# Performance work log

Measured on AMD Instinct MI355X. Metric: run time of the kernel, lower is better.

## Reference

```python
import jax, jax.numpy as jnp
import numpy as np

N_NODES = 20000
N_EDGES = 320000
IN_CH = 512
HID = 128
HEADS = 4
OUT_CH = 256
NEG_SLOPE = 0.2


def _gat_layer(x, edge_index, W, a_src, a_dst, bias, heads, out_ch, concat):
    """PyG GATConv (add_self_loops=True, eval mode: no dropout).
    x: [N, F_in], edge_index: [2, E] (row 0 = src, row 1 = dst).
    Returns (out, alpha) with alpha: [E+N, heads].
    """
    N = x.shape[0]
    h = (x @ W).reshape(N, heads, out_ch)                      # [N, H, C]
    loops = jnp.arange(N, dtype=edge_index.dtype)
    src = jnp.concatenate([edge_index[0], loops])
    dst = jnp.concatenate([edge_index[1], loops])
    a_s = jnp.einsum('nhc,hc->nh', h, a_src)                   # [N, H]
    a_d = jnp.einsum('nhc,hc->nh', h, a_dst)
    e = a_s[src] + a_d[dst]                                    # [E', H]
    e = jnp.where(e > 0, e, NEG_SLOPE * e)                     # LeakyReLU
    # segment softmax over incoming edges of each dst node
    emax = jax.ops.segment_max(e, dst, num_segments=N)
    ex = jnp.exp(e - emax[dst])
    denom = jax.ops.segment_sum(ex, dst, num_segments=N)
    alpha = ex / denom[dst]                                    # [E', H]
    msg = alpha[:, :, None] * h[src]                           # [E', H, C]
    out = jax.ops.segment_sum(msg, dst, num_segments=N)        # [N, H, C]
    out = out.reshape(N, heads * out_ch) if concat else out.mean(axis=1)
    return out + bias, alpha


def setup_inputs() -> dict:
    key = jax.random.key(0)
    ks = jax.random.split(key, 10)
    s = 0.05
    x = jax.random.normal(ks[0], (N_NODES, IN_CH), dtype=jnp.float32)
    edge_index = jax.random.randint(ks[1], (2, N_EDGES), 0, N_NODES, dtype=jnp.int32)
    W1 = jax.random.normal(ks[2], (IN_CH, HEADS * HID), dtype=jnp.float32) * s
    a_src1 = jax.random.normal(ks[3], (HEADS, HID), dtype=jnp.float32) * s
    a_dst1 = jax.random.normal(ks[4], (HEADS, HID), dtype=jnp.float32) * s
    b1 = jnp.zeros((HEADS * HID,), dtype=jnp.float32)
    W2 = jax.random.normal(ks[5], (HEADS * HID, OUT_CH), dtype=jnp.float32) * s
    a_src2 = jax.random.normal(ks[6], (1, OUT_CH), dtype=jnp.float32) * s
    a_dst2 = jax.random.normal(ks[7], (1, OUT_CH), dtype=jnp.float32) * s
    b2 = jnp.zeros((OUT_CH,), dtype=jnp.float32)
    return {"x": x, "edge_index": edge_index, "W1": W1, "a_src1": a_src1,
            "a_dst1": a_dst1, "b1": b1, "W2": W2, "a_src2": a_src2,
            "a_dst2": a_dst2, "b2": b2}


def reference(x, edge_index, W1, a_src1, a_dst1, b1, W2, a_src2, a_dst2, b2):
    h, alpha1 = _gat_layer(x, edge_index, W1, a_src1, a_dst1, b1, HEADS, HID, True)
    h = jax.nn.elu(h)
    # dropout inactive in eval mode
    out, alpha2 = _gat_layer(h, edge_index, W2, a_src2, a_dst2, b2, 1, OUT_CH, False)
    return out, alpha1, alpha2
```

## Files before the change

kernel.cpp:

```cpp
#include <hip/hip_runtime.h>
#include <hip/hip_bf16.h>
#include <cstdint>


#define NNODES 20000
#define NEDGES 320000
#define ETOT   340000
#define F1     512
#define F2     256
#define HEADS  4

typedef __bf16 bf16;
typedef __attribute__((ext_vector_type(8))) __bf16 bf16x8;
typedef __attribute__((ext_vector_type(4))) float f32x4;

__device__ __forceinline__ float bflo(unsigned p) { return __uint_as_float(p << 16); }
__device__ __forceinline__ float bfhi(unsigned p) { return __uint_as_float(p & 0xffff0000u); }

__device__ __forceinline__ void gload_lds16(const void* g, void* l) {
    __builtin_amdgcn_global_load_lds(
        (const __attribute__((address_space(1))) void*)g,
        (__attribute__((address_space(3))) void*)l, 16, 0, 0);
}

__global__ void deg_count(const int* __restrict__ ei, int* __restrict__ deg) {
    int e = blockIdx.x * blockDim.x + threadIdx.x;
    if (e >= ETOT) return;
    int dst = (e < NEDGES) ? ei[NEDGES + e] : (e - NEDGES);
    atomicAdd(&deg[dst], 1);
}

__global__ void scan_deg(const int* __restrict__ deg, int* __restrict__ offs,
                         int* __restrict__ cur) {
    __shared__ int sums[1024];
    const int t = threadIdx.x;
    const int PER = 20;
    int base = t * PER;
    int local[PER];
    int run = 0;
#pragma unroll
    for (int j = 0; j < PER; j++) {
        int i = base + j;
        int v = (i < NNODES) ? deg[i] : 0;
        local[j] = run;
        run += v;
    }
    sums[t] = run;
    __syncthreads();
    for (int o = 1; o < 1024; o <<= 1) {
        int v = (t >= o) ? sums[t - o] : 0;
        __syncthreads();
        sums[t] += v;
        __syncthreads();
    }
    int texcl = (t == 0) ? 0 : sums[t - 1];
#pragma unroll
    for (int j = 0; j < PER; j++) {
        int i = base + j;
        if (i < NNODES) {
            int e = texcl + local[j];
            cur[i] = e;
            offs[i] = e;
        }
    }
    if (t == 1023) offs[NNODES] = sums[1023];
}

__global__ void fill_csr(const int* __restrict__ ei, int* __restrict__ cur,
                         int* __restrict__ csr_src, int* __restrict__ csr_eid) {
    int e = blockIdx.x * blockDim.x + threadIdx.x;
    if (e >= ETOT) return;
    int src, dst;
    if (e < NEDGES) { src = ei[e]; dst = ei[NEDGES + e]; }
    else            { src = dst = e - NEDGES; }
    int p = atomicAdd(&cur[dst], 1);
    csr_src[p] = src;
    csr_eid[p] = e;
}

__global__ void swizzle_w(const float* __restrict__ W, bf16* __restrict__ Wh,
                          bf16* __restrict__ Wl, int K, int N) {
    int idx = blockIdx.x * blockDim.x + threadIdx.x;
    int total = (K * N) >> 3;
    if (idx >= total) return;
    int lane = idx & 63;
    int tile = idx >> 6;
    int NT = N >> 4;
    int kt = tile / NT, nt = tile - kt * NT;
    int krow = kt * 32 + (lane >> 4) * 8;
    int col  = nt * 16 + (lane & 15);
    union { bf16 b[8]; uint4 u; } hi, lo;
#pragma unroll
    for (int j = 0; j < 8; j++) {
        float w = W[(size_t)(krow + j) * N + col];
        bf16 h = (bf16)w;
        hi.b[j] = h;
        lo.b[j] = (bf16)(w - (float)h);
    }
    *(uint4*)(Wh + (size_t)idx * 8) = hi.u;
    *(uint4*)(Wl + (size_t)idx * 8) = lo.u;
}

template <int K, int N>
__global__ __launch_bounds__(256) void gemm_fused(const float* __restrict__ A,
                                                  const bf16* __restrict__ Bh,
                                                  const bf16* __restrict__ Bl,
                                                  bf16* __restrict__ Cb,
                                                  const float* __restrict__ asrc,
                                                  const float* __restrict__ adst,
                                                  float* __restrict__ as_out,
                                                  float* __restrict__ ad_out, int M) {
    __shared__ __align__(16) char smem[2][16384];
    const int lane = threadIdx.x & 63;
    const int wave = threadIdx.x >> 6;
    const int row_base = blockIdx.x * 64 + wave * 16;
    const int colt0 = blockIdx.y * 8;
    constexpr int NT = N / 16;

    const char* hbase = (const char*)Bh + (size_t)colt0 * 1024;
    const char* lbase = (const char*)Bl + (size_t)colt0 * 1024;
    auto stage = [&](int kt, int buf) {
        size_t kb = (size_t)kt * NT * 1024;
#pragma unroll
        for (int q = 0; q < 4; q++) {
            int off = wave * 4096 + q * 1024;
            const char* src = (off < 8192) ? (hbase + kb + off)
                                           : (lbase + kb + (off - 8192));
            gload_lds16(src + lane * 16, &smem[buf][off]);
        }
    };

    int arow = row_base + (lane & 15);
    if (arow >= M) arow = M - 1;
    const float* aptr = A + (size_t)arow * K + ((lane >> 4) * 8);

    f32x4 acc[8] = {};
    stage(0, 0);
    __syncthreads();
    for (int kt = 0; kt < K / 32; ++kt) {
        if (kt + 1 < K / 32) stage(kt + 1, (kt + 1) & 1);
        float av[8];
        *(float4*)(av)     = *(const float4*)(aptr + kt * 32);
        *(float4*)(av + 4) = *(const float4*)(aptr + kt * 32 + 4);
        bf16x8 ah, al;
#pragma unroll
        for (int j = 0; j < 8; j++) {
            bf16 h = (bf16)av[j];
            ah[j] = h;
            al[j] = (bf16)(av[j] - (float)h);
        }
        const char* bb = smem[kt & 1];
#pragma unroll
        for (int c = 0; c < 8; c++) {
            bf16x8 bh = *(const bf16x8*)(bb + c * 1024 + lane * 16);
            bf16x8 bl = *(const bf16x8*)(bb + 8192 + c * 1024 + lane * 16);
            acc[c] = __builtin_amdgcn_mfma_f32_16x16x32_bf16(ah, bh, acc[c], 0, 0, 0);
            acc[c] = __builtin_amdgcn_mfma_f32_16x16x32_bf16(ah, bl, acc[c], 0, 0, 0);
            acc[c] = __builtin_amdgcn_mfma_f32_16x16x32_bf16(al, bh, acc[c], 0, 0, 0);
        }
        __syncthreads();
    }

    const int crow0 = row_base + (lane >> 4) * 4;
    const int col15 = lane & 15;
#pragma unroll
    for (int c = 0; c < 8; c++)
#pragma unroll
        for (int r = 0; r < 4; r++) {
            int rr = crow0 + r;
            if (rr < M)
                Cb[(size_t)rr * N + (colt0 + c) * 16 + col15] = (bf16)acc[c][r];
        }

    float ss[4] = {}, sd[4] = {};
#pragma unroll
    for (int c = 0; c < 8; c++) {
        int cw = blockIdx.y * 128 + c * 16 + col15;
        float was = asrc[cw];
        float wad = adst[cw];
#pragma unroll
        for (int r = 0; r < 4; r++) {
            ss[r] += acc[c][r] * was;
            sd[r] += acc[c][r] * wad;
        }
    }
#pragma unroll
    for (int o = 1; o < 16; o <<= 1)
#pragma unroll
        for (int r = 0; r < 4; r++) {
            ss[r] += __shfl_xor(ss[r], o);
            sd[r] += __shfl_xor(sd[r], o);
        }
    if (col15 == 0) {
        if constexpr (N == 512) {
#pragma unroll
            for (int r = 0; r < 4; r++) {
                int rr = crow0 + r;
                if (rr < M) {
                    as_out[rr * 4 + blockIdx.y] = ss[r];
                    ad_out[rr * 4 + blockIdx.y] = sd[r];
                }
            }
        } else {
#pragma unroll
            for (int r = 0; r < 4; r++) {
                int rr = crow0 + r;
                if (rr < M) {
                    atomicAdd(&as_out[rr], ss[r]);
                    atomicAdd(&ad_out[rr], sd[r]);
                }
            }
        }
    }
}

__global__ __launch_bounds__(64) void agg1(const bf16* __restrict__ h1b,
                                           const float* __restrict__ as1,
                                           const float* __restrict__ ad1,
                                           const int* __restrict__ offs,
                                           const int* __restrict__ csr_src,
                                           const int* __restrict__ csr_eid,
                                           const float* __restrict__ b1,
                                           float* __restrict__ alpha1,
                                           float* __restrict__ h1e) {
    const int n = blockIdx.x;
    const int lane = threadIdx.x;
    const int beg = offs[n];
    const int deg = offs[n + 1] - beg;

    __shared__ int   s_src[64];
    __shared__ float s_al[64][4];

    float4 ad4 = *(const float4*)(ad1 + n * 4);
    const float adn[4] = {ad4.x, ad4.y, ad4.z, ad4.w};

    float v0[4];
    int s0 = 0, e0 = 0;
    float mx[4] = {-3e38f, -3e38f, -3e38f, -3e38f};
    for (int idx = lane; idx < deg; idx += 64) {
        int s = csr_src[beg + idx];
        float4 a4 = *(const float4*)(as1 + s * 4);
        float v[4] = {a4.x + adn[0], a4.y + adn[1], a4.z + adn[2], a4.w + adn[3]};
#pragma unroll
        for (int h = 0; h < 4; h++) {
            v[h] = v[h] > 0.f ? v[h] : 0.2f * v[h];
            mx[h] = fmaxf(mx[h], v[h]);
        }
        if (idx == lane) {
            s0 = s; e0 = csr_eid[beg + idx];
#pragma unroll
            for (int h = 0; h < 4; h++) v0[h] = v[h];
        }
    }
#pragma unroll
    for (int o = 1; o < 64; o <<= 1)
#pragma unroll
        for (int h = 0; h < 4; h++) mx[h] = fmaxf(mx[h], __shfl_xor(mx[h], o));

    float ex0[4] = {0.f, 0.f, 0.f, 0.f};
    float ls[4] = {0.f, 0.f, 0.f, 0.f};
    if (lane < deg) {
#pragma unroll
        for (int h = 0; h < 4; h++) { ex0[h] = __expf(v0[h] - mx[h]); ls[h] = ex0[h]; }
    }
    for (int idx = lane + 64; idx < deg; idx += 64) {
        int s = csr_src[beg + idx];
        float4 a4 = *(const float4*)(as1 + s * 4);
        float v[4] = {a4.x + adn[0], a4.y + adn[1], a4.z + adn[2], a4.w + adn[3]};
#pragma unroll
        for (int h = 0; h < 4; h++) {
            v[h] = v[h] > 0.f ? v[h] : 0.2f * v[h];
            ls[h] += __expf(v[h] - mx[h]);
        }
    }
#pragma unroll
    for (int o = 1; o < 64; o <<= 1)
#pragma unroll
        for (int h = 0; h < 4; h++) ls[h] += __shfl_xor(ls[h], o);
    float rden[4];
#pragma unroll
    for (int h = 0; h < 4; h++) rden[h] = 1.f / ls[h];

    float acc[8] = {};
    const int myh = lane >> 4;
    for (int base = 0; base < deg; base += 64) {
        int idx = base + lane;
        if (idx < deg) {
            int s, e;
            float al[4];
            if (base == 0) {
                s = s0; e = e0;
#pragma unroll
                for (int h = 0; h < 4; h++) al[h] = ex0[h] * rden[h];
            } else {
                s = csr_src[beg + idx];
                e = csr_eid[beg + idx];
                float4 a4 = *(const float4*)(as1 + s * 4);
                float v[4] = {a4.x + adn[0], a4.y + adn[1], a4.z + adn[2], a4.w + adn[3]};
#pragma unroll
                for (int h = 0; h < 4; h++) {
                    v[h] = v[h] > 0.f ? v[h] : 0.2f * v[h];
                    al[h] = __expf(v[h] - mx[h]) * rden[h];
                }
            }
            s_src[lane] = s;
#pragma unroll
            for (int h = 0; h < 4; h++) s_al[lane][h] = al[h];
            *(float4*)(alpha1 + (size_t)e * 4) = make_float4(al[0], al[1], al[2], al[3]);
        }
        __syncthreads();
        int cnt = min(64, deg - base);
        for (int i = 0; i < cnt; i++) {
            int s = s_src[i];
            float a = s_al[i][myh];
            uint4 p = *(const uint4*)(h1b + (size_t)s * F1 + lane * 8);
            acc[0] += a * bflo(p.x); acc[1] += a * bfhi(p.x);
            acc[2] += a * bflo(p.y); acc[3] += a * bfhi(p.y);
            acc[4] += a * bflo(p.z); acc[5] += a * bfhi(p.z);
            acc[6] += a * bflo(p.w); acc[7] += a * bfhi(p.w);
        }
        __syncthreads();
    }
    const int c8 = lane * 8;
    float bv[8];
    *(float4*)(bv)     = *(const float4*)(b1 + c8);
    *(float4*)(bv + 4) = *(const float4*)(b1 + c8 + 4);
    float o[8];
#pragma unroll
    for (int j = 0; j < 8; j++) {
        float t = acc[j] + bv[j];
        o[j] = t > 0.f ? t : expm1f(t);
    }
    *(float4*)(h1e + (size_t)n * F1 + c8)     = make_float4(o[0], o[1], o[2], o[3]);
    *(float4*)(h1e + (size_t)n * F1 + c8 + 4) = make_float4(o[4], o[5], o[6], o[7]);
}

__global__ __launch_bounds__(64) void agg2(const bf16* __restrict__ h2b,
                                           const float* __restrict__ as2,
                                           const float* __restrict__ ad2,
                                           const int* __restrict__ offs,
                                           const int* __restrict__ csr_src,
                                           const int* __restrict__ csr_eid,
                                           const float* __restrict__ b2,
                                           float* __restrict__ alpha2,
                                           float* __restrict__ out) {
    const int n = blockIdx.x;
    const int lane = threadIdx.x;
    const int beg = offs[n];
    const int deg = offs[n + 1] - beg;

    __shared__ int   s_src[64];
    __shared__ float s_al[64];

    const float adn = ad2[n];

    float v0 = 0.f;
    int s0 = 0, e0 = 0;
    float mx = -3e38f;
    for (int idx = lane; idx < deg; idx += 64) {
        int s = csr_src[beg + idx];
        float v = as2[s] + adn;
        v = v > 0.f ? v : 0.2f * v;
        mx = fmaxf(mx, v);
        if (idx == lane) { s0 = s; e0 = csr_eid[beg + idx]; v0 = v; }
    }
#pragma unroll
    for (int o = 1; o < 64; o <<= 1) mx = fmaxf(mx, __shfl_xor(mx, o));

    float ex0 = 0.f, ls = 0.f;
    if (lane < deg) { ex0 = __expf(v0 - mx); ls = ex0; }
    for (int idx = lane + 64; idx < deg; idx += 64) {
        int s = csr_src[beg + idx];
        float v = as2[s] + adn;
        v = v > 0.f ? v : 0.2f * v;
        ls += __expf(v - mx);
    }
#pragma unroll
    for (int o = 1; o < 64; o <<= 1) ls += __shfl_xor(ls, o);
    float rden = 1.f / ls;

    float acc[4] = {};
    for (int base = 0; base < deg; base += 64) {
        int idx = base + lane;
        if (idx < deg) {
            int s, e;
            float a;
            if (base == 0) { s = s0; e = e0; a = ex0 * rden; }
            else {
                s = csr_src[beg + idx];
                e = csr_eid[beg + idx];
                float v = as2[s] + adn;
                v = v > 0.f ? v : 0.2f * v;
                a = __expf(v - mx) * rden;
            }
            s_src[lane] = s;
            s_al[lane] = a;
            alpha2[e] = a;
        }
        __syncthreads();
        int cnt = min(64, deg - base);
        for (int i = 0; i < cnt; i++) {
            int s = s_src[i];
            float a = s_al[i];
            uint2 p = *(const uint2*)(h2b + (size_t)s * F2 + lane * 4);
            acc[0] += a * bflo(p.x); acc[1] += a * bfhi(p.x);
            acc[2] += a * bflo(p.y); acc[3] += a * bfhi(p.y);
        }
        __syncthreads();
    }
    const int c4 = lane * 4;
    float4 bv = *(const float4*)(b2 + c4);
    *(float4*)(out + (size_t)n * F2 + c4) =
        make_float4(acc[0] + bv.x, acc[1] + bv.y, acc[2] + bv.z, acc[3] + bv.w);
}

extern "C" void kernel_launch(void* const* d_in, const int* in_sizes, int n_in,
                              void* d_out, int out_size, void* d_ws, size_t ws_size,
                              hipStream_t stream) {
    const float* x      = (const float*)d_in[0];
    const int*   ei     = (const int*)d_in[1];
    const float* W1     = (const float*)d_in[2];
    const float* a_src1 = (const float*)d_in[3];
    const float* a_dst1 = (const float*)d_in[4];
    const float* b1     = (const float*)d_in[5];
    const float* W2     = (const float*)d_in[6];
    const float* a_src2 = (const float*)d_in[7];
    const float* a_dst2 = (const float*)d_in[8];
    const float* b2     = (const float*)d_in[9];

    char* ws = (char*)d_ws;
    size_t off = 0;
    auto alloc = [&](size_t bytes) -> char* {
        char* p = ws + off;
        off += (bytes + 255) & ~(size_t)255;
        return p;
    };
    bf16*  h1b  = (bf16*) alloc((size_t)NNODES * F1 * 2);
    bf16*  h2b  = (bf16*) alloc((size_t)NNODES * F2 * 2);
    float* h1e  = (float*)alloc((size_t)NNODES * F1 * 4);
    float* as1  = (float*)alloc((size_t)NNODES * 4 * 4);
    float* ad1  = (float*)alloc((size_t)NNODES * 4 * 4);
    float* as2  = (float*)alloc((size_t)NNODES * 4);
    float* ad2  = (float*)alloc((size_t)NNODES * 4);
    bf16*  W1h  = (bf16*) alloc((size_t)512 * 512 * 2);
    bf16*  W1l  = (bf16*) alloc((size_t)512 * 512 * 2);
    bf16*  W2h  = (bf16*) alloc((size_t)512 * 256 * 2);
    bf16*  W2l  = (bf16*) alloc((size_t)512 * 256 * 2);
    int*   deg  = (int*)  alloc((size_t)NNODES * 4);
    int*   offs = (int*)  alloc((size_t)(NNODES + 1) * 4);
    int*   cur  = (int*)  alloc((size_t)NNODES * 4);
    int*   csrS = (int*)  alloc((size_t)ETOT * 4);
    int*   csrE = (int*)  alloc((size_t)ETOT * 4);

    float* out2   = (float*)d_out;
    float* alpha1 = out2 + (size_t)NNODES * F2;
    float* alpha2 = alpha1 + (size_t)ETOT * HEADS;

    hipMemsetAsync(deg, 0, (size_t)NNODES * 4, stream);
    hipMemsetAsync(as2, 0, (size_t)NNODES * 4, stream);
    hipMemsetAsync(ad2, 0, (size_t)NNODES * 4, stream);
    deg_count<<<(ETOT + 255) / 256, 256, 0, stream>>>(ei, deg);
    scan_deg<<<1, 1024, 0, stream>>>(deg, offs, cur);
    fill_csr<<<(ETOT + 255) / 256, 256, 0, stream>>>(ei, cur, csrS, csrE);

    swizzle_w<<<(512 * 512 / 8 + 255) / 256, 256, 0, stream>>>(W1, W1h, W1l, 512, 512);
    swizzle_w<<<(512 * 256 / 8 + 255) / 256, 256, 0, stream>>>(W2, W2h, W2l, 512, 256);

    gemm_fused<512, 512><<<dim3(313, 4), 256, 0, stream>>>(
        x, W1h, W1l, h1b, a_src1, a_dst1, as1, ad1, NNODES);
    agg1<<<NNODES, 64, 0, stream>>>(h1b, as1, ad1, offs, csrS, csrE, b1, alpha1, h1e);

    gemm_fused<512, 256><<<dim3(313, 2), 256, 0, stream>>>(
        h1e, W2h, W2l, h2b, a_src2, a_dst2, as2, ad2, NNODES);
    agg2<<<NNODES, 64, 0, stream>>>(h2b, as2, ad2, offs, csrS, csrE, b2, alpha2, out2);
}
```

Before: 325.3 us.

## Pre-split A operand to bf16 hi/lo and retile GEMM to 32 rows per wave

The fp32 A operand is now split into bf16 hi/lo halves ahead of time: x gets a separate split kernel, and agg1 writes its ELU output directly as hi/lo bf16. This takes the per-tile conversion out of the GEMM inner loop. The GEMM tile changes to 128 rows by 64 columns per block, with each wave covering 32 rows so every B fragment loaded from LDS feeds two row tiles. A loads are prefetched one k-step ahead, and the attention-logit partial sums now go through atomics into zeroed buffers. The cost is an extra pass over x plus extra workspace and atomic traffic.

```diff
diff --git a/kernel.cpp b/kernel.cpp
--- a/kernel.cpp
+++ b/kernel.cpp
@@ -101,8 +101,27 @@
     *(uint4*)(Wl + (size_t)idx * 8) = lo.u;
 }
 
+__global__ void split_f32(const float* __restrict__ X, bf16* __restrict__ Xh,
+                          bf16* __restrict__ Xl, int total8) {
+    int i = blockIdx.x * blockDim.x + threadIdx.x;
+    if (i >= total8) return;
+    float v[8];
+    *(float4*)(v)     = *(const float4*)(X + (size_t)i * 8);
+    *(float4*)(v + 4) = *(const float4*)(X + (size_t)i * 8 + 4);
+    union { bf16 b[8]; uint4 u; } h, l;
+#pragma unroll
+    for (int j = 0; j < 8; j++) {
+        bf16 hh = (bf16)v[j];
+        h.b[j] = hh;
+        l.b[j] = (bf16)(v[j] - (float)hh);
+    }
+    *(uint4*)(Xh + (size_t)i * 8) = h.u;
+    *(uint4*)(Xl + (size_t)i * 8) = l.u;
+}
+
 template <int K, int N>
-__global__ __launch_bounds__(256) void gemm_fused(const float* __restrict__ A,
+__global__ __launch_bounds__(256) void gemm_fused(const bf16* __restrict__ Ah,
+                                                  const bf16* __restrict__ Al,
                                                   const bf16* __restrict__ Bh,
                                                   const bf16* __restrict__ Bl,
                                                   bf16* __restrict__ Cb,
@@ -110,105 +129,115 @@
                                                   const float* __restrict__ adst,
                                                   float* __restrict__ as_out,
                                                   float* __restrict__ ad_out, int M) {
-    __shared__ __align__(16) char smem[2][16384];
+    __shared__ __align__(16) char smem[2][8192];
     const int lane = threadIdx.x & 63;
     const int wave = threadIdx.x >> 6;
-    const int row_base = blockIdx.x * 64 + wave * 16;
-    const int colt0 = blockIdx.y * 8;
+    const int row_base = blockIdx.x * 128 + wave * 32;
+    const int colt0 = blockIdx.y * 4;
     constexpr int NT = N / 16;
+    constexpr int NKT = K / 32;
 
     const char* hbase = (const char*)Bh + (size_t)colt0 * 1024;
     const char* lbase = (const char*)Bl + (size_t)colt0 * 1024;
     auto stage = [&](int kt, int buf) {
         size_t kb = (size_t)kt * NT * 1024;
 #pragma unroll
-        for (int q = 0; q < 4; q++) {
-            int off = wave * 4096 + q * 1024;
-            const char* src = (off < 8192) ? (hbase + kb + off)
-                                           : (lbase + kb + (off - 8192));
+        for (int q = 0; q < 2; q++) {
+            int off = wave * 2048 + q * 1024;
+            const char* src = (off < 4096) ? (hbase + kb + off)
+                                           : (lbase + kb + (off - 4096));
             gload_lds16(src + lane * 16, &smem[buf][off]);
         }
     };
 
-    int arow = row_base + (lane & 15);
-    if (arow >= M) arow = M - 1;
-    const float* aptr = A + (size_t)arow * K + ((lane >> 4) * 8);
-
-    f32x4 acc[8] = {};
+    int arow0 = row_base + (lane & 15);
+    int arow1 = arow0 + 16;
+    if (arow0 >= M) arow0 = M - 1;
+    if (arow1 >= M) arow1 = M - 1;
+    const int ko = (lane >> 4) * 8;
+    const bf16* pah0 = Ah + (size_t)arow0 * K + ko;
+    const bf16* pal0 = Al + (size_t)arow0 * K + ko;
+    const bf16* pah1 = Ah + (size_t)arow1 * K + ko;
+    const bf16* pal1 = Al + (size_t)arow1 * K + ko;
+
+    f32x4 acc0[4] = {}, acc1[4] = {};
+    bf16x8 ah0 = *(const bf16x8*)pah0;
+    bf16x8 al0 = *(const bf16x8*)pal0;
+    bf16x8 ah1 = *(const bf16x8*)pah1;
+    bf16x8 al1 = *(const bf16x8*)pal1;
+
+    auto body = [&](const char* bb) {
+#pragma unroll
+        for (int c = 0; c < 4; c++) {
+            bf16x8 bh = *(const bf16x8*)(bb + c * 1024 + lane * 16);
+            bf16x8 bl = *(const bf16x8*)(bb + 4096 + c * 1024 + lane * 16);
+            acc0[c] = __builtin_amdgcn_mfma_f32_16x16x32_bf16(ah0, bh, acc0[c], 0, 0, 0);
+            acc1[c] = __builtin_amdgcn_mfma_f32_16x16x32_bf16(ah1, bh, acc1[c], 0, 0, 0);
+            acc0[c] = __builtin_amdgcn_mfma_f32_16x16x32_bf16(ah0, bl, acc0[c], 0, 0, 0);
+            acc1[c] = __builtin_amdgcn_mfma_f32_16x16x32_bf16(ah1, bl, acc1[c], 0, 0, 0);
+            acc0[c] = __builtin_amdgcn_mfma_f32_16x16x32_bf16(al0, bh, acc0[c], 0, 0, 0);
+            acc1[c] = __builtin_amdgcn_mfma_f32_16x16x32_bf16(al1, bh, acc1[c], 0, 0, 0);
+        }
+    };
+
     stage(0, 0);
     __syncthreads();
-    for (int kt = 0; kt < K / 32; ++kt) {
-        if (kt + 1 < K / 32) stage(kt + 1, (kt + 1) & 1);
-        float av[8];
-        *(float4*)(av)     = *(const float4*)(aptr + kt * 32);
-        *(float4*)(av + 4) = *(const float4*)(aptr + kt * 32 + 4);
-        bf16x8 ah, al;
-#pragma unroll
-        for (int j = 0; j < 8; j++) {
-            bf16 h = (bf16)av[j];
-            ah[j] = h;
-            al[j] = (bf16)(av[j] - (float)h);
-        }
-        const char* bb = smem[kt & 1];
-#pragma unroll
-        for (int c = 0; c < 8; c++) {
-            bf16x8 bh = *(const bf16x8*)(bb + c * 1024 + lane * 16);
-            bf16x8 bl = *(const bf16x8*)(bb + 8192 + c * 1024 + lane * 16);
-            acc[c] = __builtin_amdgcn_mfma_f32_16x16x32_bf16(ah, bh, acc[c], 0, 0, 0);
-            acc[c] = __builtin_amdgcn_mfma_f32_16x16x32_bf16(ah, bl, acc[c], 0, 0, 0);
-            acc[c] = __builtin_amdgcn_mfma_f32_16x16x32_bf16(al, bh, acc[c], 0, 0, 0);
-        }
-        __syncthreads();
-    }
+    for (int kt = 0; kt < NKT - 1; ++kt) {
+        stage(kt + 1, (kt + 1) & 1);
+        bf16x8 nah0 = *(const bf16x8*)(pah0 + (kt + 1) * 32);
+        bf16x8 nal0 = *(const bf16x8*)(pal0 + (kt + 1) * 32);
+        bf16x8 nah1 = *(const bf16x8*)(pah1 + (kt + 1) * 32);
+        bf16x8 nal1 = *(const bf16x8*)(pal1 + (kt + 1) * 32);
+        body(smem[kt & 1]);
+        __syncthreads();
+        ah0 = nah0; al0 = nal0; ah1 = nah1; al1 = nal1;
+    }
+    body(smem[(NKT - 1) & 1]);
 
     const int crow0 = row_base + (lane >> 4) * 4;
     const int col15 = lane & 15;
 #pragma unroll
-    for (int c = 0; c < 8; c++)
+    for (int c = 0; c < 4; c++)
 #pragma unroll
         for (int r = 0; r < 4; r++) {
-            int rr = crow0 + r;
-            if (rr < M)
-                Cb[(size_t)rr * N + (colt0 + c) * 16 + col15] = (bf16)acc[c][r];
-        }
-
-    float ss[4] = {}, sd[4] = {};
-#pragma unroll
-    for (int c = 0; c < 8; c++) {
-        int cw = blockIdx.y * 128 + c * 16 + col15;
+            int r0 = crow0 + r, r1 = r0 + 16;
+            int cc = (colt0 + c) * 16 + col15;
+            if (r0 < M) Cb[(size_t)r0 * N + cc] = (bf16)acc0[c][r];
+            if (r1 < M) Cb[(size_t)r1 * N + cc] = (bf16)acc1[c][r];
+        }
+
+    float ss0[4] = {}, sd0[4] = {}, ss1[4] = {}, sd1[4] = {};
+#pragma unroll
+    for (int c = 0; c < 4; c++) {
+        int cw = blockIdx.y * 64 + c * 16 + col15;
         float was = asrc[cw];
         float wad = adst[cw];
 #pragma unroll
         for (int r = 0; r < 4; r++) {
-            ss[r] += acc[c][r] * was;
-            sd[r] += acc[c][r] * wad;
+            ss0[r] += acc0[c][r] * was; sd0[r] += acc0[c][r] * wad;
+            ss1[r] += acc1[c][r] * was; sd1[r] += acc1[c][r] * wad;
         }
     }
 #pragma unroll
     for (int o = 1; o < 16; o <<= 1)
 #pragma unroll
         for (int r = 0; r < 4; r++) {
-            ss[r] += __shfl_xor(ss[r], o);
-            sd[r] += __shfl_xor(sd[r], o);
+            ss0[r] += __shfl_xor(ss0[r], o); sd0[r] += __shfl_xor(sd0[r], o);
+            ss1[r] += __shfl_xor(ss1[r], o); sd1[r] += __shfl_xor(sd1[r], o);
         }
     if (col15 == 0) {
-        if constexpr (N == 512) {
-#pragma unroll
-            for (int r = 0; r < 4; r++) {
-                int rr = crow0 + r;
-                if (rr < M) {
-                    as_out[rr * 4 + blockIdx.y] = ss[r];
-                    ad_out[rr * 4 + blockIdx.y] = sd[r];
-                }
+        constexpr int HS = (N == 512) ? 4 : 1;
+        const int head = (N == 512) ? (blockIdx.y >> 1) : 0;
+#pragma unroll
+        for (int r = 0; r < 4; r++) {
+            int r0 = crow0 + r, r1 = r0 + 16;
+            if (r0 < M) {
+                atomicAdd(&as_out[r0 * HS + head], ss0[r]);
+                atomicAdd(&ad_out[r0 * HS + head], sd0[r]);
             }
-        } else {
-#pragma unroll
-            for (int r = 0; r < 4; r++) {
-                int rr = crow0 + r;
-                if (rr < M) {
-                    atomicAdd(&as_out[rr], ss[r]);
-                    atomicAdd(&ad_out[rr], sd[r]);
-                }
+            if (r1 < M) {
+                atomicAdd(&as_out[r1 * HS + head], ss1[r]);
+                atomicAdd(&ad_out[r1 * HS + head], sd1[r]);
             }
         }
     }
@@ -222,7 +251,8 @@
                                            const int* __restrict__ csr_eid,
                                            const float* __restrict__ b1,
                                            float* __restrict__ alpha1,
-                                           float* __restrict__ h1e) {
+                                           bf16* __restrict__ h1eh,
+                                           bf16* __restrict__ h1el) {
     const int n = blockIdx.x;
     const int lane = threadIdx.x;
     const int beg = offs[n];
@@ -325,14 +355,17 @@
     float bv[8];
     *(float4*)(bv)     = *(const float4*)(b1 + c8);
     *(float4*)(bv + 4) = *(const float4*)(b1 + c8 + 4);
-    float o[8];
+    union { bf16 b[8]; uint4 u; } hh, ll;
 #pragma unroll
     for (int j = 0; j < 8; j++) {
         float t = acc[j] + bv[j];
-        o[j] = t > 0.f ? t : expm1f(t);
-    }
-    *(float4*)(h1e + (size_t)n * F1 + c8)     = make_float4(o[0], o[1], o[2], o[3]);
-    *(float4*)(h1e + (size_t)n * F1 + c8 + 4) = make_float4(o[4], o[5], o[6], o[7]);
+        float o = t > 0.f ? t : expm1f(t);
+        bf16 hb = (bf16)o;
+        hh.b[j] = hb;
+        ll.b[j] = (bf16)(o - (float)hb);
+    }
+    *(uint4*)(h1eh + (size_t)n * F1 + c8) = hh.u;
+    *(uint4*)(h1el + (size_t)n * F1 + c8) = ll.u;
 }
 
 __global__ __launch_bounds__(64) void agg2(const bf16* __restrict__ h2b,
@@ -437,7 +470,10 @@
     };
     bf16*  h1b  = (bf16*) alloc((size_t)NNODES * F1 * 2);
     bf16*  h2b  = (bf16*) alloc((size_t)NNODES * F2 * 2);
-    float* h1e  = (float*)alloc((size_t)NNODES * F1 * 4);
+    bf16*  h1eh = (bf16*) alloc((size_t)NNODES * F1 * 2);
+    bf16*  h1el = (bf16*) alloc((size_t)NNODES * F1 * 2);
+    bf16*  Xh   = (bf16*) alloc((size_t)NNODES * F1 * 2);
+    bf16*  Xl   = (bf16*) alloc((size_t)NNODES * F1 * 2);
     float* as1  = (float*)alloc((size_t)NNODES * 4 * 4);
     float* ad1  = (float*)alloc((size_t)NNODES * 4 * 4);
     float* as2  = (float*)alloc((size_t)NNODES * 4);
@@ -457,6 +493,8 @@
     float* alpha2 = alpha1 + (size_t)ETOT * HEADS;
 
     hipMemsetAsync(deg, 0, (size_t)NNODES * 4, stream);
+    hipMemsetAsync(as1, 0, (size_t)NNODES * 4 * 4, stream);
+    hipMemsetAsync(ad1, 0, (size_t)NNODES * 4 * 4, stream);
     hipMemsetAsync(as2, 0, (size_t)NNODES * 4, stream);
     hipMemsetAsync(ad2, 0, (size_t)NNODES * 4, stream);
     deg_count<<<(ETOT + 255) / 256, 256, 0, stream>>>(ei, deg);
@@ -465,12 +503,15 @@
 
     swizzle_w<<<(512 * 512 / 8 + 255) / 256, 256, 0, stream>>>(W1, W1h, W1l, 512, 512);
     swizzle_w<<<(512 * 256 / 8 + 255) / 256, 256, 0, stream>>>(W2, W2h, W2l, 512, 256);
-
-    gemm_fused<512, 512><<<dim3(313, 4), 256, 0, stream>>>(
-        x, W1h, W1l, h1b, a_src1, a_dst1, as1, ad1, NNODES);
-    agg1<<<NNODES, 64, 0, stream>>>(h1b, as1, ad1, offs, csrS, csrE, b1, alpha1, h1e);
-
-    gemm_fused<512, 256><<<dim3(313, 2), 256, 0, stream>>>(
-        h1e, W2h, W2l, h2b, a_src2, a_dst2, as2, ad2, NNODES);
+    split_f32<<<(NNODES * F1 / 8 + 255) / 256, 256, 0, stream>>>(
+        x, Xh, Xl, NNODES * F1 / 8);
+
+    gemm_fused<512, 512><<<dim3(157, 8), 256, 0, stream>>>(
+        Xh, Xl, W1h, W1l, h1b, a_src1, a_dst1, as1, ad1, NNODES);
+    agg1<<<NNODES, 64, 0, stream>>>(h1b, as1, ad1, offs, csrS, csrE, b1, alpha1,
+                                    h1eh, h1el);
+
+    gemm_fused<512, 256><<<dim3(157, 4), 256, 0, stream>>>(
+        h1eh, h1el, W2h, W2l, h2b, a_src2, a_dst2, as2, ad2, NNODES);
     agg2<<<NNODES, 64, 0, stream>>>(h2b, as2, ad2, offs, csrS, csrE, b2, alpha2, out2);
 }
```

After: 370.7 us. 14.0% more time.
